# Performance work log

Measured on AMD Instinct MI355X. Metric: run time of the kernel, lower is better.

## Reference

```python
import jax, jax.numpy as jnp
import numpy as np

H = 6            # nheads
DPH = 200.0      # dim_per_head buffer = mha_dimension / nheads (used as divisor, NOT sqrt)
EPS = 1e-5


def layernorm(x, g, b):
    m = jnp.mean(x, axis=-1, keepdims=True)
    v = jnp.mean((x - m) ** 2, axis=-1, keepdims=True)
    return (x - m) * jax.lax.rsqrt(v + EPS) * g + b


def leaky(x):
    # torch.nn.LeakyReLU(True) -> negative_slope = 1.0 (identity), kept for faithfulness
    return jnp.where(x >= 0, x, 1.0 * x)


def setup_inputs() -> dict:
    key = jax.random.key(0)
    ks = jax.random.split(key, 16)
    B, L, D, M = 4, 2048, 512, 1200
    s_in = 1.0 / np.sqrt(D)
    s_m = 1.0 / np.sqrt(M)
    return {
        "query": jax.random.normal(ks[0], (B, L, D), jnp.float32),
        "keyval": jax.random.normal(ks[1], (B, 1, D), jnp.float32),
        "Wq": jax.random.normal(ks[2], (D, M), jnp.float32) * s_in,
        "bq": jnp.zeros((M,), jnp.float32),
        "Wkv": jax.random.normal(ks[3], (D, 2 * M), jnp.float32) * s_in,
        "bkv": jnp.zeros((2 * M,), jnp.float32),
        "Wff": jax.random.normal(ks[4], (M, D), jnp.float32) * s_m,
        "bff": jnp.zeros((D,), jnp.float32),
        "g1": jnp.ones((D,), jnp.float32),
        "b1": jnp.zeros((D,), jnp.float32),
        "W2a": jax.random.normal(ks[5], (D, 4 * D), jnp.float32) * s_in,
        "b2a": jnp.zeros((4 * D,), jnp.float32),
        "W2b": jax.random.normal(ks[6], (4 * D, D), jnp.float32) / np.sqrt(4 * D),
        "b2b": jnp.zeros((D,), jnp.float32),
        "g2": jnp.ones((D,), jnp.float32),
        "b2": jnp.zeros((D,), jnp.float32),
    }


def reference(query, keyval, Wq, bq, Wkv, bkv, Wff, bff, g1, b1,
              W2a, b2a, W2b, b2b, g2, b2):
    B, L, D = query.shape
    kv = jnp.broadcast_to(keyval, query.shape)           # keyval.expand_as(query)
    Q = query @ Wq + bq                                  # [B,L,M]
    KV = kv @ Wkv + bkv                                  # [B,L,2M]
    K, V = jnp.split(KV, 2, axis=-1)

    def heads(x):  # b l (h d) -> b h l d
        return x.reshape(B, L, H, -1).transpose(0, 2, 1, 3)

    Qh, Kh, Vh = heads(Q), heads(K), heads(V)
    logits = jnp.einsum('bhid,bhjd->bhij', Qh, Kh) / DPH  # note: / d, not / sqrt(d)
    sm = jax.nn.softmax(logits, axis=-1)                  # [B,H,L,L]
    mha = jnp.einsum('bhij,bhjd->bhid', sm, Vh)
    mha_ = mha.transpose(0, 2, 1, 3).reshape(B, L, -1)    # b h i d -> b i (h d)

    out = mha_ @ Wff + bff                                # dropout = identity (eval)
    out_ = layernorm(out + query, g1, b1)
    out2 = leaky(out_ @ W2a + b2a) @ W2b + b2b
    out3 = layernorm(out_ + out2, g2, b2)
    out3 = out3 + kv
    return out3, sm
```

## Files before the change

kernel.cpp:

```cpp
#include <hip/hip_runtime.h>
#include <hip/hip_bf16.h>


typedef __bf16 bf16x8 __attribute__((ext_vector_type(8)));
typedef float f32x4 __attribute__((ext_vector_type(4)));

constexpr size_t OUT3_N = 4ull * 2048 * 512;
constexpr size_t SM_N4  = (4ull * 6 * 2048 * 2048) / 4;
constexpr float  SMV    = 1.0f / 2048.0f;

constexpr size_t S1 = 0,        C1 = 5375000;
constexpr size_t S3 = 5375000,  C3 = 5687500;
constexpr size_t S4 = 11062500, C4 = 4750000;
constexpr size_t S5 = 15812500, C5 = 5187500;
constexpr size_t S6 = 21000000, C6 = 4165824;
static_assert(S6 + C6 == SM_N4, "fill slices must cover sm");

__device__ inline void fill_slice(f32x4* __restrict__ p, size_t base, size_t cnt,
                                  int fb, int nfb){
    const f32x4 v = { SMV, SMV, SMV, SMV };
    const size_t stride = (size_t)nfb * 256;
    for (size_t j = (size_t)fb * 256 + threadIdx.x; j < cnt; j += stride)
        __builtin_nontemporal_store(v, p + base + j);
}

template<int MODE, typename OutT>
__device__ void gemm_tile(const __bf16* __restrict__ A, const __bf16* __restrict__ BT,
                          OutT* __restrict__ C, int Ndim, int Kdim,
                          int bm, int bn, int k0beg, int k0end){
    __shared__ __bf16 As[64 * 64];
    __shared__ __bf16 Bs[64 * 64];
    const int tid = threadIdx.x, wave = tid >> 6, lane = tid & 63;
    const int r_st = wave * 8 + (lane >> 3);
    const int c8g  = (lane & 7) ^ (r_st & 7);
    const __bf16* Ag = A  + (size_t)(bm + r_st) * Kdim + c8g * 8;
    const __bf16* Bg = BT + (size_t)(bn + r_st) * Kdim + c8g * 8;
    const size_t rowskip = (size_t)32 * Kdim;
    const int wm = (wave >> 1) * 32, wn = (wave & 1) * 32;
    const int lm = lane & 15, lq = lane >> 4;
    f32x4 acc[2][2] = {};
    for (int k0 = k0beg; k0 < k0end; k0 += 64){
        __builtin_amdgcn_global_load_lds(
            (const __attribute__((address_space(1))) void*)(Ag + k0),
            (__attribute__((address_space(3))) void*)&As[wave * 512], 16, 0, 0);
        __builtin_amdgcn_global_load_lds(
            (const __attribute__((address_space(1))) void*)(Ag + k0 + rowskip),
            (__attribute__((address_space(3))) void*)&As[2048 + wave * 512], 16, 0, 0);
        __builtin_amdgcn_global_load_lds(
            (const __attribute__((address_space(1))) void*)(Bg + k0),
            (__attribute__((address_space(3))) void*)&Bs[wave * 512], 16, 0, 0);
        __builtin_amdgcn_global_load_lds(
            (const __attribute__((address_space(1))) void*)(Bg + k0 + rowskip),
            (__attribute__((address_space(3))) void*)&Bs[2048 + wave * 512], 16, 0, 0);
        __syncthreads();
        #pragma unroll
        for (int kb = 0; kb < 64; kb += 32){
            const int sw = (((kb >> 3) + lq) ^ (lm & 7)) << 3;
            bf16x8 a0 = *(const bf16x8*)&As[(wm + lm) * 64 + sw];
            bf16x8 a1 = *(const bf16x8*)&As[(wm + 16 + lm) * 64 + sw];
            bf16x8 b0 = *(const bf16x8*)&Bs[(wn + lm) * 64 + sw];
            bf16x8 b1 = *(const bf16x8*)&Bs[(wn + 16 + lm) * 64 + sw];
            acc[0][0] = __builtin_amdgcn_mfma_f32_16x16x32_bf16(a0, b0, acc[0][0], 0, 0, 0);
            acc[0][1] = __builtin_amdgcn_mfma_f32_16x16x32_bf16(a0, b1, acc[0][1], 0, 0, 0);
            acc[1][0] = __builtin_amdgcn_mfma_f32_16x16x32_bf16(a1, b0, acc[1][0], 0, 0, 0);
            acc[1][1] = __builtin_amdgcn_mfma_f32_16x16x32_bf16(a1, b1, acc[1][1], 0, 0, 0);
        }
        __syncthreads();
    }
    #pragma unroll
    for (int mi = 0; mi < 2; ++mi)
      #pragma unroll
      for (int ni = 0; ni < 2; ++ni)
        #pragma unroll
        for (int r = 0; r < 4; ++r){
            int row = bm + wm + mi * 16 + lq * 4 + r;
            int col = bn + wn + ni * 16 + lm;
            if (MODE == 1)      atomicAdd((float*)&C[(size_t)row * Ndim + col], acc[mi][ni][r]);
            else if (MODE == 2) C[(size_t)row * Ndim + col] = (OutT)acc[mi][ni][r];
            else                C[(size_t)row * Ndim + col] = (OutT)acc[mi][ni][r];
        }
}

__global__ __launch_bounds__(256) void k1_prep_kv(const float* __restrict__ W2a,
        const float* __restrict__ b2a, __bf16* __restrict__ A1,
        const float* __restrict__ W2b, __bf16* __restrict__ W2bT,
        const float* __restrict__ keyval, const float* __restrict__ Wkv,
        const float* __restrict__ bkv, float* __restrict__ V, f32x4* __restrict__ smf){
    __shared__ float sh[32 * 33];
    const int bid = blockIdx.x, tid = threadIdx.x;
    if (bid < 1152){
        int r = bid >> 1;
        int c = (bid & 1) * 1024 + tid * 4;
        float4 v;
        if (r < 512)       v = *(const float4*)(W2a + (size_t)r * 2048 + c);
        else if (r == 512) v = *(const float4*)(b2a + c);
        else               v = make_float4(0.f, 0.f, 0.f, 0.f);
        __bf16* o = A1 + (size_t)r * 2048 + c;
        o[0] = (__bf16)v.x; o[1] = (__bf16)v.y; o[2] = (__bf16)v.z; o[3] = (__bf16)v.w;
    } else if (bid < 2176){
        int t = bid - 1152;
        int c0 = (t & 15) * 32, r0 = (t >> 4) * 32;
        int tx = tid & 31, ty = tid >> 5;
        for (int i = ty; i < 32; i += 8)
            sh[i * 33 + tx] = W2b[(size_t)(r0 + i) * 512 + c0 + tx];
        __syncthreads();
        for (int i = ty; i < 32; i += 8)
            W2bT[(size_t)(c0 + i) * 2048 + r0 + tx] = (__bf16)sh[tx * 33 + i];
    } else if (bid < 2336){
        int i = bid - 2176;
        int b = i & 3, mc = (i >> 2) % 5, kc = i / 20;
        int m = mc * 256 + tid;
        if (m < 1200){
            float acc = (kc == 0) ? bkv[1200 + m] : 0.f;
            const float* kvb = keyval + (size_t)b * 512;
            int d0 = kc * 64;
            #pragma unroll 8
            for (int d = d0; d < d0 + 64; ++d)
                acc += kvb[d] * Wkv[(size_t)d * 2400 + 1200 + m];
            atomicAdd(&V[b * 1200 + m], acc);
        }
    } else {
        fill_slice(smf, S1, C1, bid - 2336, 512);
    }
}

__global__ __launch_bounds__(256) void k3_fold_oc(const __bf16* __restrict__ A1,
        const __bf16* __restrict__ W2bT, float* __restrict__ Wf,
        const float* __restrict__ V, const float* __restrict__ Wff,
        const float* __restrict__ bff, float* __restrict__ oc, f32x4* __restrict__ smf){
    const int bid = blockIdx.x, tid = threadIdx.x;
    if (bid < 288){
        int tile = bid % 72, kc = bid / 72;
        gemm_tile<1>(A1, W2bT, Wf, 512, 2048, (tile % 9) * 64, (tile / 9) * 64,
                     kc * 512, (kc + 1) * 512);
    } else if (bid < 384){
        int i = bid - 288;
        int b = i & 3, jc = (i >> 2) & 1, kc = i >> 3;
        int j = jc * 256 + tid;
        float acc = (kc == 0) ? bff[j] : 0.f;
        const float* vb = V + b * 1200;
        int m0 = kc * 100;
        #pragma unroll 5
        for (int m = m0; m < m0 + 100; ++m)
            acc += vb[m] * Wff[(size_t)m * 512 + j];
        atomicAdd(&oc[b * 512 + j], acc);
    } else {
        fill_slice(smf, S3, C3, bid - 384, 512);
    }
}

__global__ __launch_bounds__(256) void k4_ln1_tcast(const float* __restrict__ q,
        const float* __restrict__ oc, const float* __restrict__ g1,
        const float* __restrict__ b1, __bf16* __restrict__ Xb,
        const float* __restrict__ Wf, __bf16* __restrict__ WfT, f32x4* __restrict__ smf){
    __shared__ float sh[32 * 33];
    const int bid = blockIdx.x, t = threadIdx.x;
    if (bid < 8192){
        const int b = bid >> 11;
        const size_t base = (size_t)bid * 512;
        float2 qv = *(const float2*)(q + base + 2 * t);
        float2 ov = *(const float2*)(oc + (size_t)b * 512 + 2 * t);
        float v0 = qv.x + ov.x, v1 = qv.y + ov.y;
        float s = v0 + v1, ss = v0 * v0 + v1 * v1;
        for (int off = 32; off; off >>= 1){ s += __shfl_down(s, off); ss += __shfl_down(ss, off); }
        int wv = t >> 6, ln = t & 63;
        if (ln == 0){ sh[wv] = s; sh[4 + wv] = ss; }
        __syncthreads();
        if (t == 0){
            float S  = sh[0] + sh[1] + sh[2] + sh[3];
            float SS = sh[4] + sh[5] + sh[6] + sh[7];
            float m = S * (1.0f / 512.0f);
            float var = SS * (1.0f / 512.0f) - m * m;
            sh[0] = m; sh[1] = rsqrtf(var + 1e-5f);
        }
        __syncthreads();
        float m = sh[0], r = sh[1];
        float2 gv = *(const float2*)(g1 + 2 * t);
        float2 bv = *(const float2*)(b1 + 2 * t);
        union { __bf16 h[2]; unsigned u; } pk;
        pk.h[0] = (__bf16)((v0 - m) * r * gv.x + bv.x);
        pk.h[1] = (__bf16)((v1 - m) * r * gv.y + bv.y);
        *(unsigned*)(Xb + base + 2 * t) = pk.u;
    } else if (bid < 8448){
        int tt = bid - 8192;
        int c0 = (tt & 15) * 32, r0 = (tt >> 4) * 32;
        int tx = t & 31, ty = t >> 5;
        for (int i = ty; i < 32; i += 8)
            sh[i * 33 + tx] = Wf[(size_t)(r0 + i) * 512 + c0 + tx];
        __syncthreads();
        for (int i = ty; i < 32; i += 8)
            WfT[(size_t)(c0 + i) * 512 + r0 + tx] = (__bf16)sh[tx * 33 + i];
    } else {
        fill_slice(smf, S4, C4, bid - 8448, 512);
    }
}

__global__ __launch_bounds__(256) void k5_gemm(const __bf16* __restrict__ X,
        const __bf16* __restrict__ WfT, __bf16* __restrict__ out2, f32x4* __restrict__ smf){
    const int bid = blockIdx.x;
    if (bid < 1024){
        gemm_tile<2>(X, WfT, out2, 512, 512, (bid >> 3) * 64, (bid & 7) * 64, 0, 512);
    } else {
        fill_slice(smf, S5, C5, bid - 1024, 512);
    }
}

__global__ __launch_bounds__(256) void k6_ln2(const __bf16* __restrict__ X,
        const __bf16* __restrict__ o2, const float* __restrict__ bfrow,
        const float* __restrict__ b2b, const float* __restrict__ g2,
        const float* __restrict__ b2, const float* __restrict__ keyval,
        float* __restrict__ out3, f32x4* __restrict__ smf){
    __shared__ float sh[8];
    const int bid = blockIdx.x, t = threadIdx.x;
    if (bid < 8192){
        const int b = bid >> 11;
        const size_t base = (size_t)bid * 512;
        union { unsigned u; __bf16 h[2]; } xv, yv;
        xv.u = *(const unsigned*)(X + base + 2 * t);
        yv.u = *(const unsigned*)(o2 + base + 2 * t);
        float f0 = bfrow[2 * t] + b2b[2 * t], f1 = bfrow[2 * t + 1] + b2b[2 * t + 1];
        float v0 = (float)xv.h[0] + (float)yv.h[0] + f0;
        float v1 = (float)xv.h[1] + (float)yv.h[1] + f1;
        float s = v0 + v1, ss = v0 * v0 + v1 * v1;
        for (int off = 32; off; off >>= 1){ s += __shfl_down(s, off); ss += __shfl_down(ss, off); }
        int wv = t >> 6, ln = t & 63;
        if (ln == 0){ sh[wv] = s; sh[4 + wv] = ss; }
        __syncthreads();
        if (t == 0){
            float S  = sh[0] + sh[1] + sh[2] + sh[3];
            float SS = sh[4] + sh[5] + sh[6] + sh[7];
            float m = S * (1.0f / 512.0f);
            float var = SS * (1.0f / 512.0f) - m * m;
            sh[0] = m; sh[1] = rsqrtf(var + 1e-5f);
        }
        __syncthreads();
        float m = sh[0], r = sh[1];
        float2 gv = *(const float2*)(g2 + 2 * t);
        float2 bv = *(const float2*)(b2 + 2 * t);
        float2 kv = *(const float2*)(keyval + (size_t)b * 512 + 2 * t);
        float y0 = (v0 - m) * r * gv.x + bv.x + kv.x;
        float y1 = (v1 - m) * r * gv.y + bv.y + kv.y;
        *(float2*)(out3 + base + 2 * t) = make_float2(y0, y1);
    } else {
        fill_slice(smf, S6, C6, bid - 8192, 512);
    }
}

extern "C" void kernel_launch(void* const* d_in, const int* in_sizes, int n_in,
                              void* d_out, int out_size, void* d_ws, size_t ws_size,
                              hipStream_t stream){
    const float* query  = (const float*)d_in[0];
    const float* keyval = (const float*)d_in[1];
    const float* Wkv = (const float*)d_in[4];
    const float* bkv = (const float*)d_in[5];
    const float* Wff = (const float*)d_in[6];
    const float* bff = (const float*)d_in[7];
    const float* g1  = (const float*)d_in[8];
    const float* b1  = (const float*)d_in[9];
    const float* W2a = (const float*)d_in[10];
    const float* b2a = (const float*)d_in[11];
    const float* W2b = (const float*)d_in[12];
    const float* b2b = (const float*)d_in[13];
    const float* g2  = (const float*)d_in[14];
    const float* b2  = (const float*)d_in[15];

    float* out3 = (float*)d_out;
    f32x4* smf  = (f32x4*)(out3 + OUT3_N);

    char* base = (ws_size >= (64ull << 20)) ? (char*)d_ws : (char*)smf;
    float*  t_Wf   = (float*)base;
    float*  t_V    = t_Wf + 294912;
    float*  t_oc   = t_V + 4800;
    __bf16* t_A1   = (__bf16*)(t_oc + 2048);
    __bf16* t_W2bT = t_A1 + 1179648;
    __bf16* t_WfT  = t_W2bT + 1048576;
    __bf16* t_X    = t_WfT + 262144;
    __bf16* t_out2 = t_X + 4194304;

    (void)hipMemsetAsync(t_Wf, 0, 301760 * sizeof(float), stream);
    k1_prep_kv<<<2848, 256, 0, stream>>>(W2a, b2a, t_A1, W2b, t_W2bT,
                                         keyval, Wkv, bkv, t_V, smf);
    k3_fold_oc<<<896, 256, 0, stream>>>(t_A1, t_W2bT, t_Wf, t_V, Wff, bff, t_oc, smf);
    k4_ln1_tcast<<<8960, 256, 0, stream>>>(query, t_oc, g1, b1, t_X, t_Wf, t_WfT, smf);
    k5_gemm<<<1536, 256, 0, stream>>>(t_X, t_WfT, t_out2, smf);
    k6_ln2<<<8704, 256, 0, stream>>>(t_X, t_out2, t_Wf + 262144, b2b, g2, b2,
                                     keyval, out3, smf);
}
```

Baseline: 496.2 us.

## Fuse all stages into one cooperative persistent kernel with grid syncs

```diff
diff --git a/kernel.cpp b/kernel.cpp
--- a/kernel.cpp
+++ b/kernel.cpp
@@ -1,5 +1,8 @@
 #include <hip/hip_runtime.h>
 #include <hip/hip_bf16.h>
+#include <hip/hip_cooperative_groups.h>
+
+namespace cg = cooperative_groups;
 
 
 typedef __bf16 bf16x8 __attribute__((ext_vector_type(8)));
@@ -16,8 +19,8 @@
 constexpr size_t S6 = 21000000, C6 = 4165824;
 static_assert(S6 + C6 == SM_N4, "fill slices must cover sm");
 
-__device__ inline void fill_slice(f32x4* __restrict__ p, size_t base, size_t cnt,
-                                  int fb, int nfb){
+__device__ __forceinline__ void fill_slice(f32x4* __restrict__ p, size_t base, size_t cnt,
+                                           int fb, int nfb){
     const f32x4 v = { SMV, SMV, SMV, SMV };
     const size_t stride = (size_t)nfb * 256;
     for (size_t j = (size_t)fb * 256 + threadIdx.x; j < cnt; j += stride)
@@ -75,39 +78,39 @@
         for (int r = 0; r < 4; ++r){
             int row = bm + wm + mi * 16 + lq * 4 + r;
             int col = bn + wn + ni * 16 + lm;
-            if (MODE == 1)      atomicAdd((float*)&C[(size_t)row * Ndim + col], acc[mi][ni][r]);
-            else if (MODE == 2) C[(size_t)row * Ndim + col] = (OutT)acc[mi][ni][r];
-            else                C[(size_t)row * Ndim + col] = (OutT)acc[mi][ni][r];
+            if (MODE == 1) atomicAdd((float*)&C[(size_t)row * Ndim + col], acc[mi][ni][r]);
+            else           C[(size_t)row * Ndim + col] = (OutT)acc[mi][ni][r];
         }
 }
 
-__global__ __launch_bounds__(256) void k1_prep_kv(const float* __restrict__ W2a,
+
+__device__ __forceinline__ void item_p1(int item, const float* __restrict__ W2a,
         const float* __restrict__ b2a, __bf16* __restrict__ A1,
         const float* __restrict__ W2b, __bf16* __restrict__ W2bT,
         const float* __restrict__ keyval, const float* __restrict__ Wkv,
-        const float* __restrict__ bkv, float* __restrict__ V, f32x4* __restrict__ smf){
-    __shared__ float sh[32 * 33];
-    const int bid = blockIdx.x, tid = threadIdx.x;
-    if (bid < 1152){
-        int r = bid >> 1;
-        int c = (bid & 1) * 1024 + tid * 4;
+        const float* __restrict__ bkv, float* __restrict__ V, float* __restrict__ shT){
+    const int tid = threadIdx.x;
+    if (item < 1152){
+        int r = item >> 1;
+        int c = (item & 1) * 1024 + tid * 4;
         float4 v;
         if (r < 512)       v = *(const float4*)(W2a + (size_t)r * 2048 + c);
         else if (r == 512) v = *(const float4*)(b2a + c);
         else               v = make_float4(0.f, 0.f, 0.f, 0.f);
         __bf16* o = A1 + (size_t)r * 2048 + c;
         o[0] = (__bf16)v.x; o[1] = (__bf16)v.y; o[2] = (__bf16)v.z; o[3] = (__bf16)v.w;
-    } else if (bid < 2176){
-        int t = bid - 1152;
+    } else if (item < 2176){
+        int t = item - 1152;
         int c0 = (t & 15) * 32, r0 = (t >> 4) * 32;
         int tx = tid & 31, ty = tid >> 5;
         for (int i = ty; i < 32; i += 8)
-            sh[i * 33 + tx] = W2b[(size_t)(r0 + i) * 512 + c0 + tx];
+            shT[i * 33 + tx] = W2b[(size_t)(r0 + i) * 512 + c0 + tx];
         __syncthreads();
         for (int i = ty; i < 32; i += 8)
-            W2bT[(size_t)(c0 + i) * 2048 + r0 + tx] = (__bf16)sh[tx * 33 + i];
-    } else if (bid < 2336){
-        int i = bid - 2176;
+            W2bT[(size_t)(c0 + i) * 2048 + r0 + tx] = (__bf16)shT[tx * 33 + i];
+        __syncthreads();
+    } else {
+        int i = item - 2176;
         int b = i & 3, mc = (i >> 2) % 5, kc = i / 20;
         int m = mc * 256 + tid;
         if (m < 1200){
@@ -119,22 +122,20 @@
                 acc += kvb[d] * Wkv[(size_t)d * 2400 + 1200 + m];
             atomicAdd(&V[b * 1200 + m], acc);
         }
-    } else {
-        fill_slice(smf, S1, C1, bid - 2336, 512);
-    }
-}
-
-__global__ __launch_bounds__(256) void k3_fold_oc(const __bf16* __restrict__ A1,
+    }
+}
+
+__device__ __forceinline__ void item_p2(int item, const __bf16* __restrict__ A1,
         const __bf16* __restrict__ W2bT, float* __restrict__ Wf,
         const float* __restrict__ V, const float* __restrict__ Wff,
-        const float* __restrict__ bff, float* __restrict__ oc, f32x4* __restrict__ smf){
-    const int bid = blockIdx.x, tid = threadIdx.x;
-    if (bid < 288){
-        int tile = bid % 72, kc = bid / 72;
+        const float* __restrict__ bff, float* __restrict__ oc){
+    const int tid = threadIdx.x;
+    if (item < 288){
+        int tile = item % 72, kc = item / 72;
         gemm_tile<1>(A1, W2bT, Wf, 512, 2048, (tile % 9) * 64, (tile / 9) * 64,
                      kc * 512, (kc + 1) * 512);
-    } else if (bid < 384){
-        int i = bid - 288;
+    } else {
+        int i = item - 288;
         int b = i & 3, jc = (i >> 2) & 1, kc = i >> 3;
         int j = jc * 256 + tid;
         float acc = (kc == 0) ? bff[j] : 0.f;
@@ -144,106 +145,158 @@
         for (int m = m0; m < m0 + 100; ++m)
             acc += vb[m] * Wff[(size_t)m * 512 + j];
         atomicAdd(&oc[b * 512 + j], acc);
-    } else {
-        fill_slice(smf, S3, C3, bid - 384, 512);
-    }
-}
-
-__global__ __launch_bounds__(256) void k4_ln1_tcast(const float* __restrict__ q,
+    }
+}
+
+__device__ __forceinline__ void item_p3(int item, const float* __restrict__ q,
         const float* __restrict__ oc, const float* __restrict__ g1,
         const float* __restrict__ b1, __bf16* __restrict__ Xb,
-        const float* __restrict__ Wf, __bf16* __restrict__ WfT, f32x4* __restrict__ smf){
-    __shared__ float sh[32 * 33];
-    const int bid = blockIdx.x, t = threadIdx.x;
-    if (bid < 8192){
-        const int b = bid >> 11;
-        const size_t base = (size_t)bid * 512;
+        const float* __restrict__ Wf, __bf16* __restrict__ WfT, float* __restrict__ shT){
+    const int t = threadIdx.x;
+    if (item < 8192){
+        const int b = item >> 11;
+        const size_t base = (size_t)item * 512;
         float2 qv = *(const float2*)(q + base + 2 * t);
         float2 ov = *(const float2*)(oc + (size_t)b * 512 + 2 * t);
         float v0 = qv.x + ov.x, v1 = qv.y + ov.y;
         float s = v0 + v1, ss = v0 * v0 + v1 * v1;
         for (int off = 32; off; off >>= 1){ s += __shfl_down(s, off); ss += __shfl_down(ss, off); }
         int wv = t >> 6, ln = t & 63;
-        if (ln == 0){ sh[wv] = s; sh[4 + wv] = ss; }
+        if (ln == 0){ shT[wv] = s; shT[4 + wv] = ss; }
         __syncthreads();
         if (t == 0){
-            float S  = sh[0] + sh[1] + sh[2] + sh[3];
-            float SS = sh[4] + sh[5] + sh[6] + sh[7];
+            float S  = shT[0] + shT[1] + shT[2] + shT[3];
+            float SS = shT[4] + shT[5] + shT[6] + shT[7];
             float m = S * (1.0f / 512.0f);
             float var = SS * (1.0f / 512.0f) - m * m;
-            sh[0] = m; sh[1] = rsqrtf(var + 1e-5f);
+            shT[0] = m; shT[1] = rsqrtf(var + 1e-5f);
         }
         __syncthreads();
-        float m = sh[0], r = sh[1];
+        float m = shT[0], r = shT[1];
         float2 gv = *(const float2*)(g1 + 2 * t);
         float2 bv = *(const float2*)(b1 + 2 * t);
         union { __bf16 h[2]; unsigned u; } pk;
         pk.h[0] = (__bf16)((v0 - m) * r * gv.x + bv.x);
         pk.h[1] = (__bf16)((v1 - m) * r * gv.y + bv.y);
         *(unsigned*)(Xb + base + 2 * t) = pk.u;
-    } else if (bid < 8448){
-        int tt = bid - 8192;
+        __syncthreads();
+    } else {
+        int tt = item - 8192;
         int c0 = (tt & 15) * 32, r0 = (tt >> 4) * 32;
         int tx = t & 31, ty = t >> 5;
         for (int i = ty; i < 32; i += 8)
-            sh[i * 33 + tx] = Wf[(size_t)(r0 + i) * 512 + c0 + tx];
+            shT[i * 33 + tx] = Wf[(size_t)(r0 + i) * 512 + c0 + tx];
         __syncthreads();
         for (int i = ty; i < 32; i += 8)
-            WfT[(size_t)(c0 + i) * 512 + r0 + tx] = (__bf16)sh[tx * 33 + i];
-    } else {
-        fill_slice(smf, S4, C4, bid - 8448, 512);
-    }
-}
-
-__global__ __launch_bounds__(256) void k5_gemm(const __bf16* __restrict__ X,
-        const __bf16* __restrict__ WfT, __bf16* __restrict__ out2, f32x4* __restrict__ smf){
-    const int bid = blockIdx.x;
-    if (bid < 1024){
-        gemm_tile<2>(X, WfT, out2, 512, 512, (bid >> 3) * 64, (bid & 7) * 64, 0, 512);
-    } else {
-        fill_slice(smf, S5, C5, bid - 1024, 512);
-    }
-}
-
-__global__ __launch_bounds__(256) void k6_ln2(const __bf16* __restrict__ X,
+            WfT[(size_t)(c0 + i) * 512 + r0 + tx] = (__bf16)shT[tx * 33 + i];
+        __syncthreads();
+    }
+}
+
+__device__ __forceinline__ void item_p5(int item, const __bf16* __restrict__ X,
         const __bf16* __restrict__ o2, const float* __restrict__ bfrow,
         const float* __restrict__ b2b, const float* __restrict__ g2,
         const float* __restrict__ b2, const float* __restrict__ keyval,
-        float* __restrict__ out3, f32x4* __restrict__ smf){
-    __shared__ float sh[8];
-    const int bid = blockIdx.x, t = threadIdx.x;
-    if (bid < 8192){
-        const int b = bid >> 11;
-        const size_t base = (size_t)bid * 512;
-        union { unsigned u; __bf16 h[2]; } xv, yv;
-        xv.u = *(const unsigned*)(X + base + 2 * t);
-        yv.u = *(const unsigned*)(o2 + base + 2 * t);
-        float f0 = bfrow[2 * t] + b2b[2 * t], f1 = bfrow[2 * t + 1] + b2b[2 * t + 1];
-        float v0 = (float)xv.h[0] + (float)yv.h[0] + f0;
-        float v1 = (float)xv.h[1] + (float)yv.h[1] + f1;
-        float s = v0 + v1, ss = v0 * v0 + v1 * v1;
-        for (int off = 32; off; off >>= 1){ s += __shfl_down(s, off); ss += __shfl_down(ss, off); }
-        int wv = t >> 6, ln = t & 63;
-        if (ln == 0){ sh[wv] = s; sh[4 + wv] = ss; }
-        __syncthreads();
-        if (t == 0){
-            float S  = sh[0] + sh[1] + sh[2] + sh[3];
-            float SS = sh[4] + sh[5] + sh[6] + sh[7];
-            float m = S * (1.0f / 512.0f);
-            float var = SS * (1.0f / 512.0f) - m * m;
-            sh[0] = m; sh[1] = rsqrtf(var + 1e-5f);
-        }
-        __syncthreads();
-        float m = sh[0], r = sh[1];
-        float2 gv = *(const float2*)(g2 + 2 * t);
-        float2 bv = *(const float2*)(b2 + 2 * t);
-        float2 kv = *(const float2*)(keyval + (size_t)b * 512 + 2 * t);
-        float y0 = (v0 - m) * r * gv.x + bv.x + kv.x;
-        float y1 = (v1 - m) * r * gv.y + bv.y + kv.y;
-        *(float2*)(out3 + base + 2 * t) = make_float2(y0, y1);
-    } else {
-        fill_slice(smf, S6, C6, bid - 8192, 512);
-    }
+        float* __restrict__ out3, float* __restrict__ shT){
+    const int t = threadIdx.x;
+    const int b = item >> 11;
+    const size_t base = (size_t)item * 512;
+    union { unsigned u; __bf16 h[2]; } xv, yv;
+    xv.u = *(const unsigned*)(X + base + 2 * t);
+    yv.u = *(const unsigned*)(o2 + base + 2 * t);
+    float f0 = bfrow[2 * t] + b2b[2 * t], f1 = bfrow[2 * t + 1] + b2b[2 * t + 1];
+    float v0 = (float)xv.h[0] + (float)yv.h[0] + f0;
+    float v1 = (float)xv.h[1] + (float)yv.h[1] + f1;
+    float s = v0 + v1, ss = v0 * v0 + v1 * v1;
+    for (int off = 32; off; off >>= 1){ s += __shfl_down(s, off); ss += __shfl_down(ss, off); }
+    int wv = t >> 6, ln = t & 63;
+    if (ln == 0){ shT[wv] = s; shT[4 + wv] = ss; }
+    __syncthreads();
+    if (t == 0){
+        float S  = shT[0] + shT[1] + shT[2] + shT[3];
+        float SS = shT[4] + shT[5] + shT[6] + shT[7];
+        float m = S * (1.0f / 512.0f);
+        float var = SS * (1.0f / 512.0f) - m * m;
+        shT[0] = m; shT[1] = rsqrtf(var + 1e-5f);
+    }
+    __syncthreads();
+    float m = shT[0], r = shT[1];
+    float2 gv = *(const float2*)(g2 + 2 * t);
+    float2 bv = *(const float2*)(b2 + 2 * t);
+    float2 kv = *(const float2*)(keyval + (size_t)b * 512 + 2 * t);
+    float y0 = (v0 - m) * r * gv.x + bv.x + kv.x;
+    float y1 = (v1 - m) * r * gv.y + bv.y + kv.y;
+    *(float2*)(out3 + base + 2 * t) = make_float2(y0, y1);
+    __syncthreads();
+}
+
+__global__ __launch_bounds__(256) void fused(const float* query, const float* keyval,
+        const float* Wkv, const float* bkv, const float* Wff, const float* bff,
+        const float* g1, const float* b1, const float* W2a, const float* b2a,
+        const float* W2b, const float* b2b, const float* g2, const float* b2,
+        float* out3, f32x4* smf, float* Wf, float* V, float* oc,
+        __bf16* A1, __bf16* W2bT, __bf16* WfT, __bf16* X, __bf16* out2){
+    __shared__ float shT[32 * 33];
+    cg::grid_group g = cg::this_grid();
+    const int nb = gridDim.x, bid = blockIdx.x;
+    for (size_t i = (size_t)bid * 256 + threadIdx.x; i < 75440; i += (size_t)nb * 256)
+        ((f32x4*)Wf)[i] = (f32x4){0.f, 0.f, 0.f, 0.f};
+    g.sync();
+    for (int item = bid; item < 2336; item += nb)
+        item_p1(item, W2a, b2a, A1, W2b, W2bT, keyval, Wkv, bkv, V, shT);
+    fill_slice(smf, S1, C1, bid, nb);
+    g.sync();
+    for (int item = bid; item < 384; item += nb)
+        item_p2(item, A1, W2bT, Wf, V, Wff, bff, oc);
+    fill_slice(smf, S3, C3, bid, nb);
+    g.sync();
+    for (int item = bid; item < 8448; item += nb)
+        item_p3(item, query, oc, g1, b1, X, Wf, WfT, shT);
+    fill_slice(smf, S4, C4, bid, nb);
+    g.sync();
+    for (int item = bid; item < 1024; item += nb)
+        gemm_tile<2>(X, WfT, out2, 512, 512, (item >> 3) * 64, (item & 7) * 64, 0, 512);
+    fill_slice(smf, S5, C5, bid, nb);
+    g.sync();
+    for (int item = bid; item < 8192; item += nb)
+        item_p5(item, X, out2, Wf + 262144, b2b, g2, b2, keyval, out3, shT);
+    fill_slice(smf, S6, C6, bid, nb);
+}
+
+__global__ __launch_bounds__(256) void w1(const float* W2a, const float* b2a, __bf16* A1,
+        const float* W2b, __bf16* W2bT, const float* keyval, const float* Wkv,
+        const float* bkv, float* V, f32x4* smf){
+    __shared__ float shT[32 * 33];
+    const int bid = blockIdx.x;
+    if (bid < 2336) item_p1(bid, W2a, b2a, A1, W2b, W2bT, keyval, Wkv, bkv, V, shT);
+    else            fill_slice(smf, S1, C1, bid - 2336, 512);
+}
+__global__ __launch_bounds__(256) void w2(const __bf16* A1, const __bf16* W2bT, float* Wf,
+        const float* V, const float* Wff, const float* bff, float* oc, f32x4* smf){
+    const int bid = blockIdx.x;
+    if (bid < 384) item_p2(bid, A1, W2bT, Wf, V, Wff, bff, oc);
+    else           fill_slice(smf, S3, C3, bid - 384, 512);
+}
+__global__ __launch_bounds__(256) void w3(const float* q, const float* oc, const float* g1,
+        const float* b1, __bf16* X, const float* Wf, __bf16* WfT, f32x4* smf){
+    __shared__ float shT[32 * 33];
+    const int bid = blockIdx.x;
+    if (bid < 8448) item_p3(bid, q, oc, g1, b1, X, Wf, WfT, shT);
+    else            fill_slice(smf, S4, C4, bid - 8448, 512);
+}
+__global__ __launch_bounds__(256) void w4(const __bf16* X, const __bf16* WfT,
+        __bf16* out2, f32x4* smf){
+    const int bid = blockIdx.x;
+    if (bid < 1024) gemm_tile<2>(X, WfT, out2, 512, 512, (bid >> 3) * 64, (bid & 7) * 64, 0, 512);
+    else            fill_slice(smf, S5, C5, bid - 1024, 512);
+}
+__global__ __launch_bounds__(256) void w5(const __bf16* X, const __bf16* out2,
+        const float* bfrow, const float* b2b, const float* g2, const float* b2,
+        const float* keyval, float* out3, f32x4* smf){
+    __shared__ float shT[32 * 33];
+    const int bid = blockIdx.x;
+    if (bid < 8192) item_p5(bid, X, out2, bfrow, b2b, g2, b2, keyval, out3, shT);
+    else            fill_slice(smf, S6, C6, bid - 8192, 512);
 }
 
 extern "C" void kernel_launch(void* const* d_in, const int* in_sizes, int n_in,
@@ -277,12 +330,21 @@
     __bf16* t_X    = t_WfT + 262144;
     __bf16* t_out2 = t_X + 4194304;
 
-    (void)hipMemsetAsync(t_Wf, 0, 301760 * sizeof(float), stream);
-    k1_prep_kv<<<2848, 256, 0, stream>>>(W2a, b2a, t_A1, W2b, t_W2bT,
-                                         keyval, Wkv, bkv, t_V, smf);
-    k3_fold_oc<<<896, 256, 0, stream>>>(t_A1, t_W2bT, t_Wf, t_V, Wff, bff, t_oc, smf);
-    k4_ln1_tcast<<<8960, 256, 0, stream>>>(query, t_oc, g1, b1, t_X, t_Wf, t_WfT, smf);
-    k5_gemm<<<1536, 256, 0, stream>>>(t_X, t_WfT, t_out2, smf);
-    k6_ln2<<<8704, 256, 0, stream>>>(t_X, t_out2, t_Wf + 262144, b2b, g2, b2,
-                                     keyval, out3, smf);
-}
+    void* args[] = {
+        (void*)&query, (void*)&keyval, (void*)&Wkv, (void*)&bkv, (void*)&Wff,
+        (void*)&bff, (void*)&g1, (void*)&b1, (void*)&W2a, (void*)&b2a,
+        (void*)&W2b, (void*)&b2b, (void*)&g2, (void*)&b2,
+        (void*)&out3, (void*)&smf, (void*)&t_Wf, (void*)&t_V, (void*)&t_oc,
+        (void*)&t_A1, (void*)&t_W2bT, (void*)&t_WfT, (void*)&t_X, (void*)&t_out2
+    };
+    hipError_t err = hipLaunchCooperativeKernel((const void*)fused, dim3(512), dim3(256),
+                                                args, 0, stream);
+    if (err != hipSuccess){
+        (void)hipMemsetAsync(t_Wf, 0, 301760 * sizeof(float), stream);
+        w1<<<2848, 256, 0, stream>>>(W2a, b2a, t_A1, W2b, t_W2bT, keyval, Wkv, bkv, t_V, smf);
+        w2<<<896, 256, 0, stream>>>(t_A1, t_W2bT, t_Wf, t_V, Wff, bff, t_oc, smf);
+        w3<<<8960, 256, 0, stream>>>(query, t_oc, g1, b1, t_X, t_Wf, t_WfT, smf);
+        w4<<<1536, 256, 0, stream>>>(t_X, t_WfT, t_out2, smf);
+        w5<<<8704, 256, 0, stream>>>(t_X, t_out2, t_Wf + 262144, b2b, g2, b2, keyval, out3, smf);
+    }
+}
```

New measurement: 872.8 us. 1.76x slower.
